# Performance work log

Measured on AMD Instinct MI355X. Metric: run time of the kernel, lower is better.

The kernel has to match this reference:

```python
import jax, jax.numpy as jnp
import numpy as np

N = 12000
E = 384000
NEG_SLOPE = 0.2


def add_self_loops(edge_index, n):
    loops = jnp.arange(n, dtype=edge_index.dtype)
    return jnp.concatenate([edge_index, jnp.stack([loops, loops])], axis=1)


def gat_conv(x, edge_index, W, a_src, a_dst, b, n):
    # PyG GATConv, heads=1, concat=True, add_self_loops=True
    h = x @ W                      # [N, F_out]
    ei = add_self_loops(edge_index, n)
    src, dst = ei[0], ei[1]
    alpha_s = h @ a_src            # [N]
    alpha_d = h @ a_dst            # [N]
    e = jax.nn.leaky_relu(alpha_s[src] + alpha_d[dst], NEG_SLOPE)  # [E+N]
    # segment softmax over incoming edges of each dst node
    m = jax.ops.segment_max(e, dst, num_segments=n)
    ex = jnp.exp(e - m[dst])
    s = jax.ops.segment_sum(ex, dst, num_segments=n)
    alpha = ex / s[dst]
    out = jax.ops.segment_sum(alpha[:, None] * h[src], dst, num_segments=n)
    return out + b


def setup_inputs() -> dict:
    key = jax.random.key(0)
    ks = jax.random.split(key, 10)
    x = jax.random.normal(ks[0], (N, 40), dtype=jnp.float32)
    edge_index = jax.random.randint(ks[1], (2, E), 0, N, dtype=jnp.int64)
    sc1 = 1.0 / np.sqrt(40.0)
    sc2 = 1.0 / np.sqrt(50.0)
    return {
        "x": x,
        "edge_index": edge_index,
        "W1": jax.random.normal(ks[2], (40, 50), dtype=jnp.float32) * sc1,
        "a_src1": jax.random.normal(ks[3], (50,), dtype=jnp.float32) * sc2,
        "a_dst1": jax.random.normal(ks[4], (50,), dtype=jnp.float32) * sc2,
        "b1": jnp.zeros((50,), dtype=jnp.float32),
        "W2": jax.random.normal(ks[5], (50, 40), dtype=jnp.float32) * sc2,
        "a_src2": jax.random.normal(ks[6], (40,), dtype=jnp.float32) * sc1,
        "a_dst2": jax.random.normal(ks[7], (40,), dtype=jnp.float32) * sc1,
        "b2": jnp.zeros((40,), dtype=jnp.float32),
    }


def reference(x, edge_index, W1, a_src1, a_dst1, b1, W2, a_src2, a_dst2, b2):
    h = jax.nn.relu(gat_conv(x, edge_index, W1, a_src1, a_dst1, b1, N))
    z = jax.nn.relu(gat_conv(h, edge_index, W2, a_src2, a_dst2, b2, N))
    adj_pred = jax.nn.sigmoid(z @ z.T)   # [N, N] inner-product decoder
    return adj_pred
```

## Files before the change

kernel.cpp:

```cpp
#include <hip/hip_runtime.h>
#include <cstdint>
#include <cstddef>

#define N_NODES 12000
#define N_EDGES 384000
#define NEG_SLOPE 0.2f

__device__ __forceinline__ float leaky(float v) { return v > 0.f ? v : NEG_SLOPE * v; }

template <int FIN, int FOUT>
__global__ __launch_bounds__(256) void node_linear(
    const float* __restrict__ x, const float* __restrict__ W,
    const float* __restrict__ a_src, const float* __restrict__ a_dst,
    float* __restrict__ h, float* __restrict__ as_, float* __restrict__ ad_) {
  __shared__ float Ws[FIN * FOUT];
  __shared__ float av[FOUT], dv[FOUT];
  for (int i = threadIdx.x; i < FIN * FOUT; i += blockDim.x) Ws[i] = W[i];
  if (threadIdx.x < FOUT) {
    av[threadIdx.x] = a_src[threadIdx.x];
    dv[threadIdx.x] = a_dst[threadIdx.x];
  }
  __syncthreads();
  const int node = blockIdx.x * blockDim.x + threadIdx.x;
  if (node >= N_NODES) return;
  float xr[FIN];
#pragma unroll
  for (int k = 0; k < FIN; ++k) xr[k] = x[node * FIN + k];
  float ssum = 0.f, dsum = 0.f;
#pragma unroll 1
  for (int c = 0; c < FOUT; ++c) {
    float acc = 0.f;
#pragma unroll
    for (int k = 0; k < FIN; ++k) acc += xr[k] * Ws[k * FOUT + c];
    h[node * FOUT + c] = acc;
    ssum += acc * av[c];
    dsum += acc * dv[c];
  }
  as_[node] = ssum;
  ad_[node] = dsum;
}

__global__ __launch_bounds__(256) void histo_kernel(const int* __restrict__ dst,
                                                    int* __restrict__ deg) {
  const int i = blockIdx.x * blockDim.x + threadIdx.x;
  if (i >= N_EDGES + N_NODES) return;
  const int d = (i < N_EDGES) ? dst[i] : (i - N_EDGES);
  atomicAdd(&deg[d], 1);
}

__global__ __launch_bounds__(1024) void scan_kernel(const int* __restrict__ deg,
                                                    int* __restrict__ rowp) {
  __shared__ int wsum[16];
  __shared__ int carry_s;
  const int t = threadIdx.x;
  const int lane = t & 63;
  const int w = t >> 6;
  if (t == 0) carry_s = 0;
  __syncthreads();
  for (int base = 0; base < N_NODES; base += 1024) {
    const int idx = base + t;
    const int v = (idx < N_NODES) ? deg[idx] : 0;
    int run = v;
#pragma unroll
    for (int off = 1; off < 64; off <<= 1) {
      const int u = __shfl_up(run, off);
      if (lane >= off) run += u;
    }
    if (lane == 63) wsum[w] = run;
    __syncthreads();
    if (w == 0) {
      int x = (lane < 16) ? wsum[lane] : 0;
#pragma unroll
      for (int off = 1; off < 16; off <<= 1) {
        const int u = __shfl_up(x, off);
        if (lane >= off) x += u;
      }
      if (lane < 16) wsum[lane] = x;
    }
    __syncthreads();
    const int wpre = (w == 0) ? 0 : wsum[w - 1];
    const int c = carry_s;
    if (idx < N_NODES) rowp[idx] = c + wpre + run - v;
    __syncthreads();
    if (t == 1023) carry_s = c + wsum[15];
    __syncthreads();
  }
  if (t == 0) rowp[N_NODES] = carry_s;
}

__global__ __launch_bounds__(256) void scatter_kernel(
    const int* __restrict__ src, const int* __restrict__ dst,
    const int* __restrict__ rowp, int* __restrict__ fill,
    int* __restrict__ esrc) {
  const int i = blockIdx.x * blockDim.x + threadIdx.x;
  if (i >= N_EDGES + N_NODES) return;
  int s, d;
  if (i < N_EDGES) {
    s = src[i];
    d = dst[i];
  } else {
    s = d = i - N_EDGES;
  }
  const int pos = rowp[d] + atomicAdd(&fill[d], 1);
  esrc[pos] = s;
}

template <int F>
__global__ __launch_bounds__(256) void gat_aggregate(
    const int* __restrict__ rowp, const int* __restrict__ esrc,
    const float* __restrict__ h, const float* __restrict__ as_,
    const float* __restrict__ ad_, const float* __restrict__ b,
    float* __restrict__ out) {
  __shared__ float wc[4][128];
  __shared__ int sc[4][128];
  const int ws = threadIdx.x >> 6;
  const int wid = (blockIdx.x * blockDim.x + threadIdx.x) >> 6;
  const int lane = threadIdx.x & 63;
  if (wid >= N_NODES) return;
  const int start = rowp[wid], end = rowp[wid + 1];
  const float adv = ad_[wid];

  int s0 = 0, s1 = 0;
  float e0 = -1e30f, e1 = -1e30f;
  const int i0 = start + lane, i1 = start + 64 + lane;
  if (i0 < end) { s0 = esrc[i0]; e0 = leaky(as_[s0] + adv); }
  if (i1 < end) { s1 = esrc[i1]; e1 = leaky(as_[s1] + adv); }
  float m = fmaxf(e0, e1);
  for (int i = start + 128 + lane; i < end; i += 64)
    m = fmaxf(m, leaky(as_[esrc[i]] + adv));
#pragma unroll
  for (int off = 32; off; off >>= 1) m = fmaxf(m, __shfl_xor(m, off));

  const float w0 = (i0 < end) ? __expf(e0 - m) : 0.f;
  const float w1 = (i1 < end) ? __expf(e1 - m) : 0.f;
  float ssum = w0 + w1;
  for (int i = start + 128 + lane; i < end; i += 64)
    ssum += __expf(leaky(as_[esrc[i]] + adv) - m);
#pragma unroll
  for (int off = 32; off; off >>= 1) ssum += __shfl_xor(ssum, off);
  const float inv = 1.f / ssum;

  sc[ws][lane] = s0;
  sc[ws][lane + 64] = s1;
  wc[ws][lane] = w0;
  wc[ws][lane + 64] = w1;

  const int deg = end - start;
  const int ncached = deg < 128 ? deg : 128;
  float acc = 0.f, acc2 = 0.f;
  int j = 0;
  for (; j + 1 < ncached; j += 2) {
    const int t0 = sc[ws][j], t1 = sc[ws][j + 1];
    const float u0 = wc[ws][j], u1 = wc[ws][j + 1];
    if (lane < F) {
      acc += u0 * h[t0 * F + lane];
      acc2 += u1 * h[t1 * F + lane];
    }
  }
  for (; j < ncached; ++j)
    if (lane < F) acc += wc[ws][j] * h[sc[ws][j] * F + lane];
  for (int i = start + 128; i < end; ++i) {
    const int s = esrc[i];
    const float w = __expf(leaky(as_[s] + adv) - m);
    if (lane < F) acc += w * h[s * F + lane];
  }
  if (lane < F) {
    const float o = (acc + acc2) * inv + b[lane];
    out[wid * F + lane] = o > 0.f ? o : 0.f;
  }
}

__global__ __launch_bounds__(256) void decoder_kernel(const float* __restrict__ z,
                                                      float* __restrict__ out) {
  const int bx = blockIdx.x, by = blockIdx.y;
  if (bx > by) return;
  __shared__ float At[40][132];
  __shared__ float Bt[40][132];
  const int i0 = by * 128;
  const int j0 = bx * 128;
  const int t = threadIdx.x;

  for (int u = t; u < 1280; u += 256) {
    const int row = u / 10;
    const int kq = u - row * 10;
    int ga = i0 + row;
    ga = ga < N_NODES ? ga : N_NODES - 1;
    const float4 va = *(const float4*)(z + ga * 40 + kq * 4);
    At[kq * 4 + 0][row] = va.x;
    At[kq * 4 + 1][row] = va.y;
    At[kq * 4 + 2][row] = va.z;
    At[kq * 4 + 3][row] = va.w;
    int gb = j0 + row;
    gb = gb < N_NODES ? gb : N_NODES - 1;
    const float4 vb = *(const float4*)(z + gb * 40 + kq * 4);
    Bt[kq * 4 + 0][row] = vb.x;
    Bt[kq * 4 + 1][row] = vb.y;
    Bt[kq * 4 + 2][row] = vb.z;
    Bt[kq * 4 + 3][row] = vb.w;
  }
  __syncthreads();

  const int tx = t & 15, ty = t >> 4;
  float acc[8][8] = {};
  for (int k = 0; k < 40; ++k) {
    float a[8], b[8];
    *(float4*)&a[0] = *(const float4*)&At[k][ty * 8];
    *(float4*)&a[4] = *(const float4*)&At[k][ty * 8 + 4];
    *(float4*)&b[0] = *(const float4*)&Bt[k][tx * 8];
    *(float4*)&b[4] = *(const float4*)&Bt[k][tx * 8 + 4];
#pragma unroll
    for (int r = 0; r < 8; ++r)
#pragma unroll
      for (int c = 0; c < 8; ++c) acc[r][c] += a[r] * b[c];
  }

#pragma unroll
  for (int r = 0; r < 8; ++r)
#pragma unroll
    for (int c = 0; c < 8; ++c) acc[r][c] = 1.0f / (1.0f + __expf(-acc[r][c]));

#pragma unroll
  for (int r = 0; r < 8; ++r) {
    const int gi = i0 + ty * 8 + r;
    if (gi < N_NODES) {
      const int gj = j0 + tx * 8;
      float* dstp = out + (size_t)gi * N_NODES + gj;
      if (gj + 7 < N_NODES) {
        *(float4*)dstp = make_float4(acc[r][0], acc[r][1], acc[r][2], acc[r][3]);
        *(float4*)(dstp + 4) = make_float4(acc[r][4], acc[r][5], acc[r][6], acc[r][7]);
      } else {
#pragma unroll
        for (int c = 0; c < 8; ++c)
          if (gj + c < N_NODES) dstp[c] = acc[r][c];
      }
    }
  }

  if (bx < by) {
#pragma unroll
    for (int c = 0; c < 8; ++c) {
      const int gr = j0 + tx * 8 + c;
      const int ci = i0 + ty * 8;
      float* dstp = out + (size_t)gr * N_NODES + ci;
      if (ci + 7 < N_NODES) {
        *(float4*)dstp = make_float4(acc[0][c], acc[1][c], acc[2][c], acc[3][c]);
        *(float4*)(dstp + 4) = make_float4(acc[4][c], acc[5][c], acc[6][c], acc[7][c]);
      } else {
#pragma unroll
        for (int r = 0; r < 8; ++r)
          if (ci + r < N_NODES) dstp[r] = acc[r][c];
      }
    }
  }
}

extern "C" void kernel_launch(void* const* d_in, const int* in_sizes, int n_in,
                              void* d_out, int out_size, void* d_ws, size_t ws_size,
                              hipStream_t stream) {
  const float* x     = (const float*)d_in[0];
  const int*   ei    = (const int*)d_in[1];
  const float* W1    = (const float*)d_in[2];
  const float* asrc1 = (const float*)d_in[3];
  const float* adst1 = (const float*)d_in[4];
  const float* b1    = (const float*)d_in[5];
  const float* W2    = (const float*)d_in[6];
  const float* asrc2 = (const float*)d_in[7];
  const float* adst2 = (const float*)d_in[8];
  const float* b2    = (const float*)d_in[9];
  float* out = (float*)d_out;

  float* wsp  = (float*)d_ws;
  float* h1   = wsp;
  float* out1 = h1 + 600000;
  float* h2   = out1 + 600000;
  float* z    = h2 + 480000;
  float* as_  = z + 480000;
  float* ad_  = as_ + 12000;
  int* deg  = (int*)(ad_ + 12000);
  int* fill = deg + 12000;
  int* rowp = fill + 12000;
  int* esrc = rowp + 12001;

  const int* src = ei;
  const int* dst = ei + N_EDGES;

  hipMemsetAsync(deg, 0, 2 * N_NODES * sizeof(int), stream);

  const int eb = (N_EDGES + N_NODES + 255) / 256;
  histo_kernel<<<eb, 256, 0, stream>>>(dst, deg);
  scan_kernel<<<1, 1024, 0, stream>>>(deg, rowp);
  scatter_kernel<<<eb, 256, 0, stream>>>(src, dst, rowp, fill, esrc);

  const int nb = (N_NODES + 255) / 256;
  node_linear<40, 50><<<nb, 256, 0, stream>>>(x, W1, asrc1, adst1, h1, as_, ad_);
  gat_aggregate<50><<<3000, 256, 0, stream>>>(rowp, esrc, h1, as_, ad_, b1, out1);
  node_linear<50, 40><<<nb, 256, 0, stream>>>(out1, W2, asrc2, adst2, h2, as_, ad_);
  gat_aggregate<40><<<3000, 256, 0, stream>>>(rowp, esrc, h2, as_, ad_, b2, z);

  dim3 dgrid(94, 94);
  decoder_kernel<<<dgrid, 256, 0, stream>>>(z, out);
}
```

Baseline: 793.7 us.

## Compute decoder Gram matrix with split-bf16 MFMA over triangular tile grid

```diff
diff --git a/kernel.cpp b/kernel.cpp
--- a/kernel.cpp
+++ b/kernel.cpp
@@ -5,6 +5,11 @@
 #define N_NODES 12000
 #define N_EDGES 384000
 #define NEG_SLOPE 0.2f
+#define NPAD 12032
+#define KP 64
+
+typedef __attribute__((ext_vector_type(8))) short bf16x8;
+typedef __attribute__((ext_vector_type(4))) float f32x4;
 
 __device__ __forceinline__ float leaky(float v) { return v > 0.f ? v : NEG_SLOPE * v; }
 
@@ -170,85 +175,87 @@
   }
 }
 
-__global__ __launch_bounds__(256) void decoder_kernel(const float* __restrict__ z,
-                                                      float* __restrict__ out) {
-  const int bx = blockIdx.x, by = blockIdx.y;
-  if (bx > by) return;
-  __shared__ float At[40][132];
-  __shared__ float Bt[40][132];
-  const int i0 = by * 128;
-  const int j0 = bx * 128;
-  const int t = threadIdx.x;
-
-  for (int u = t; u < 1280; u += 256) {
-    const int row = u / 10;
-    const int kq = u - row * 10;
-    int ga = i0 + row;
-    ga = ga < N_NODES ? ga : N_NODES - 1;
-    const float4 va = *(const float4*)(z + ga * 40 + kq * 4);
-    At[kq * 4 + 0][row] = va.x;
-    At[kq * 4 + 1][row] = va.y;
-    At[kq * 4 + 2][row] = va.z;
-    At[kq * 4 + 3][row] = va.w;
-    int gb = j0 + row;
-    gb = gb < N_NODES ? gb : N_NODES - 1;
-    const float4 vb = *(const float4*)(z + gb * 40 + kq * 4);
-    Bt[kq * 4 + 0][row] = vb.x;
-    Bt[kq * 4 + 1][row] = vb.y;
-    Bt[kq * 4 + 2][row] = vb.z;
-    Bt[kq * 4 + 3][row] = vb.w;
-  }
-  __syncthreads();
-
-  const int tx = t & 15, ty = t >> 4;
-  float acc[8][8] = {};
-  for (int k = 0; k < 40; ++k) {
-    float a[8], b[8];
-    *(float4*)&a[0] = *(const float4*)&At[k][ty * 8];
-    *(float4*)&a[4] = *(const float4*)&At[k][ty * 8 + 4];
-    *(float4*)&b[0] = *(const float4*)&Bt[k][tx * 8];
-    *(float4*)&b[4] = *(const float4*)&Bt[k][tx * 8 + 4];
-#pragma unroll
-    for (int r = 0; r < 8; ++r)
-#pragma unroll
-      for (int c = 0; c < 8; ++c) acc[r][c] += a[r] * b[c];
-  }
-
-#pragma unroll
-  for (int r = 0; r < 8; ++r)
-#pragma unroll
-    for (int c = 0; c < 8; ++c) acc[r][c] = 1.0f / (1.0f + __expf(-acc[r][c]));
-
-#pragma unroll
-  for (int r = 0; r < 8; ++r) {
-    const int gi = i0 + ty * 8 + r;
-    if (gi < N_NODES) {
-      const int gj = j0 + tx * 8;
-      float* dstp = out + (size_t)gi * N_NODES + gj;
-      if (gj + 7 < N_NODES) {
-        *(float4*)dstp = make_float4(acc[r][0], acc[r][1], acc[r][2], acc[r][3]);
-        *(float4*)(dstp + 4) = make_float4(acc[r][4], acc[r][5], acc[r][6], acc[r][7]);
-      } else {
-#pragma unroll
-        for (int c = 0; c < 8; ++c)
-          if (gj + c < N_NODES) dstp[c] = acc[r][c];
-      }
-    }
-  }
-
-  if (bx < by) {
-#pragma unroll
-    for (int c = 0; c < 8; ++c) {
-      const int gr = j0 + tx * 8 + c;
-      const int ci = i0 + ty * 8;
-      float* dstp = out + (size_t)gr * N_NODES + ci;
-      if (ci + 7 < N_NODES) {
-        *(float4*)dstp = make_float4(acc[0][c], acc[1][c], acc[2][c], acc[3][c]);
-        *(float4*)(dstp + 4) = make_float4(acc[4][c], acc[5][c], acc[6][c], acc[7][c]);
-      } else {
-#pragma unroll
-        for (int r = 0; r < 8; ++r)
-          if (ci + r < N_NODES) dstp[r] = acc[r][c];
+__global__ __launch_bounds__(256) void split_bf16(const float* __restrict__ z,
+                                                  short* __restrict__ zh,
+                                                  short* __restrict__ zl) {
+  const int idx = blockIdx.x * 256 + threadIdx.x;
+  if (idx >= NPAD * KP) return;
+  const int row = idx >> 6, k = idx & (KP - 1);
+  float v = 0.f;
+  if (row < N_NODES && k < 40) v = z[row * 40 + k];
+  const unsigned u = __float_as_uint(v);
+  const unsigned hb = (u + 0x7fffu + ((u >> 16) & 1u)) >> 16;
+  const float hf = __uint_as_float(hb << 16);
+  const float r = v - hf;
+  const unsigned ur = __float_as_uint(r);
+  const unsigned lb = (ur + 0x7fffu + ((ur >> 16) & 1u)) >> 16;
+  zh[idx] = (short)hb;
+  zl[idx] = (short)lb;
+}
+
+__global__ __launch_bounds__(256) void decoder_mfma(const short* __restrict__ zh,
+                                                    const short* __restrict__ zl,
+                                                    float* __restrict__ out) {
+  const int p = blockIdx.x;
+  int by = (int)((sqrtf(8.f * (float)p + 1.f) - 1.f) * 0.5f);
+  while ((by + 1) * (by + 2) / 2 <= p) ++by;
+  while (by * (by + 1) / 2 > p) --by;
+  const int bx = p - by * (by + 1) / 2;
+  const int i0 = by * 128, j0 = bx * 128;
+  const int w = threadIdx.x >> 6, l = threadIdx.x & 63;
+  const int lr = l & 15;
+  const int koff = (l >> 4) * 8;
+
+  bf16x8 Ah[2][2], Al[2][2];
+  const int arow = i0 + w * 32 + lr;
+#pragma unroll
+  for (int rt = 0; rt < 2; ++rt)
+#pragma unroll
+    for (int s = 0; s < 2; ++s) {
+      const size_t off = (size_t)(arow + rt * 16) * KP + s * 32 + koff;
+      Ah[rt][s] = *(const bf16x8*)(zh + off);
+      Al[rt][s] = *(const bf16x8*)(zl + off);
+    }
+
+#pragma unroll
+  for (int ct = 0; ct < 8; ++ct) {
+    const size_t boff = (size_t)(j0 + ct * 16 + lr) * KP + koff;
+    const bf16x8 Bh0 = *(const bf16x8*)(zh + boff);
+    const bf16x8 Bh1 = *(const bf16x8*)(zh + boff + 32);
+    const bf16x8 Bl0 = *(const bf16x8*)(zl + boff);
+    const bf16x8 Bl1 = *(const bf16x8*)(zl + boff + 32);
+#pragma unroll
+    for (int rt = 0; rt < 2; ++rt) {
+      f32x4 c = {0.f, 0.f, 0.f, 0.f};
+      c = __builtin_amdgcn_mfma_f32_16x16x32_bf16(Ah[rt][0], Bh0, c, 0, 0, 0);
+      c = __builtin_amdgcn_mfma_f32_16x16x32_bf16(Ah[rt][1], Bh1, c, 0, 0, 0);
+      c = __builtin_amdgcn_mfma_f32_16x16x32_bf16(Ah[rt][0], Bl0, c, 0, 0, 0);
+      c = __builtin_amdgcn_mfma_f32_16x16x32_bf16(Ah[rt][1], Bl1, c, 0, 0, 0);
+      c = __builtin_amdgcn_mfma_f32_16x16x32_bf16(Al[rt][0], Bh0, c, 0, 0, 0);
+      c = __builtin_amdgcn_mfma_f32_16x16x32_bf16(Al[rt][1], Bh1, c, 0, 0, 0);
+
+      float o[4];
+#pragma unroll
+      for (int j = 0; j < 4; ++j) o[j] = 1.f / (1.f + __expf(-c[j]));
+
+      const int gi0 = i0 + w * 32 + rt * 16 + (l >> 4) * 4;
+      const int gj = j0 + ct * 16 + lr;
+      if (gj < N_NODES) {
+#pragma unroll
+        for (int j = 0; j < 4; ++j) {
+          const int gi = gi0 + j;
+          if (gi < N_NODES) out[(size_t)gi * N_NODES + gj] = o[j];
+        }
+        if (bx < by) {
+          float* dstp = out + (size_t)gj * N_NODES + gi0;
+          if (gi0 + 3 < N_NODES) {
+            *(float4*)dstp = make_float4(o[0], o[1], o[2], o[3]);
+          } else {
+#pragma unroll
+            for (int j = 0; j < 4; ++j)
+              if (gi0 + j < N_NODES) dstp[j] = o[j];
+          }
+        }
       }
     }
   }
@@ -280,6 +287,8 @@
   int* fill = deg + 12000;
   int* rowp = fill + 12000;
   int* esrc = rowp + 12001;
+  short* zh = (short*)(esrc + 396004);
+  short* zl = zh + NPAD * KP;
 
   const int* src = ei;
   const int* dst = ei + N_EDGES;
@@ -297,6 +306,8 @@
   node_linear<50, 40><<<nb, 256, 0, stream>>>(out1, W2, asrc2, adst2, h2, as_, ad_);
   gat_aggregate<40><<<3000, 256, 0, stream>>>(rowp, esrc, h2, as_, ad_, b2, z);
 
-  dim3 dgrid(94, 94);
-  decoder_kernel<<<dgrid, 256, 0, stream>>>(z, out);
-}
+  split_bf16<<<(NPAD * KP + 255) / 256, 256, 0, stream>>>(z, zh, zl);
+
+  const int tri = (94 * 95) / 2;
+  decoder_mfma<<<tri, 256, 0, stream>>>(zh, zl, out);
+}
```

Measured after the change: 852.9 us. 7.5% more time.
